# Optimization experiments

Measured on AMD Instinct MI355X. Metric: run time of the kernel, lower is better.

## Reference

```python
import jax, jax.numpy as jnp
import numpy as np

N_DIMS = 8
N_REGIMES = 8
CAPACITY = 16
KERNEL = 2
DILATIONS = (1, 2, 4, 8)
BOTTLE = (32, 32, 32, 32)
B = 128
T_LEN = 512
N_STEPS = T_LEN - CAPACITY


def setup_inputs() -> dict:
    key = jax.random.key(0)
    ks = jax.random.split(key, 8)
    x = jax.random.normal(ks[0], (B, N_DIMS, T_LEN), jnp.float32)
    temp = jnp.ones((), jnp.float32)
    u = jax.random.uniform(ks[1], (N_STEPS, B, 1, N_REGIMES), jnp.float32)

    def mkw(k, o, i):
        return jax.random.normal(k, (o, i, KERNEL), jnp.float32) / np.float32(np.sqrt(i * KERNEL))

    c_in = N_DIMS + N_REGIMES
    w0 = mkw(ks[2], BOTTLE[0], c_in)
    b0 = jnp.zeros((BOTTLE[0],), jnp.float32)
    w1 = mkw(ks[3], BOTTLE[1], BOTTLE[0])
    b1 = jnp.zeros((BOTTLE[1],), jnp.float32)
    w2 = mkw(ks[4], BOTTLE[2], BOTTLE[1])
    b2 = jnp.zeros((BOTTLE[2],), jnp.float32)
    w3 = mkw(ks[5], N_REGIMES, BOTTLE[3])
    b3 = jnp.zeros((N_REGIMES,), jnp.float32)
    return {"x": x, "temp": temp, "u": u, "w0": w0, "b0": b0, "w1": w1,
            "b1": b1, "w2": w2, "b2": b2, "w3": w3, "b3": b3, "T": T_LEN}


def _conv(h, w, b, d):
    # causal dilated conv1d, VALID padding (windowing handles causality)
    out = jax.lax.conv_general_dilated(h, w, (1,), 'VALID', rhs_dilation=(d,),
                                       dimension_numbers=('NCH', 'OIH', 'NCH'))
    return out + b[None, :, None]


def _forward(x, temp, u, params, T):
    cap = CAPACITY
    pad = sum(DILATIONS)  # F.pad(x, (sum(dilations), 0)) -> left-pad time axis
    xpad = jnp.pad(x, ((0, 0), (0, 0), (pad, 0)))
    n_steps = T - cap
    # windows x_pad[:, :, t-cap:t] for t in [cap, T) -> (n_steps, B, D, cap)
    idx = jnp.arange(n_steps)[:, None] + jnp.arange(cap)[None, :]
    xw = jnp.transpose(xpad[:, :, idx], (2, 0, 1, 3))
    g = -jnp.log(-jnp.log(u + 1e-10) + 1e-10)  # Gumbel(0,1) noise
    Bn = x.shape[0]
    K = u.shape[-1]
    z0 = jnp.zeros((Bn, K, cap), x.dtype)  # capacity initial zero regimes
    layers = tuple(zip(params[0::2], params[1::2], DILATIONS))

    def step(zbuf, inp):
        xw_t, g_t = inp  # (B, D, cap), (B, 1, K)
        h = jnp.concatenate([xw_t, zbuf], axis=1)  # (B, D+K, cap)
        for (w, b, d) in layers:
            h = jax.nn.elu(_conv(h, w, b, d))
        logq = jax.nn.log_softmax(h[:, :, -1], axis=1)  # (B, K)
        y = jax.nn.softmax((logq + g_t[:, 0, :]) / temp, axis=-1)  # gumbel-softmax sample
        zbuf = jnp.concatenate([zbuf[:, :, 1:], y[:, :, None]], axis=2)
        return zbuf, (y, logq)

    _, (zs, logqs) = jax.lax.scan(step, z0, (xw, g))
    z_all = jnp.concatenate([z0, jnp.transpose(zs, (1, 2, 0))], axis=2)  # (B, K, T)
    logq_out = jnp.transpose(logqs, (1, 2, 0))[..., None]  # (B, K, n_steps, 1) = torch.stack(dim=2)
    return z_all, logq_out


def reference(x, temp, u, w0, b0, w1, b1, w2, b2, w3, b3, T):
    return _forward(x, temp, u, (w0, b0, w1, b1, w2, b2, w3, b3), T)
```

## Files before the change

kernel.cpp:

```cpp
#include <hip/hip_runtime.h>

#define NB      128
#define ND      8
#define NK      8
#define TLEN    512
#define NSTEPS  496

#define INVLN2f 1.44269504088896340736f

__device__ __forceinline__ float fexp(float x) { return __expf(x); }
__device__ __forceinline__ float flog(float x) { return __logf(x); }
__device__ __forceinline__ float frcp(float x) { return __builtin_amdgcn_rcpf(x); }
__device__ __forceinline__ float elur(float x) { return x > 0.f ? x : fexp(x) - 1.f; }

#if defined(__has_builtin)
#if __has_builtin(__builtin_amdgcn_exp2f)
#define fexp2(x) __builtin_amdgcn_exp2f(x)
#endif
#endif
#ifndef fexp2
#define fexp2(x) exp2f(x)
#endif

#define DPP_ROR4(v) __int_as_float(__builtin_amdgcn_mov_dpp(__float_as_int(v), 0x124, 0xF, 0xF, false))
#define DPP_X1(v)   __int_as_float(__builtin_amdgcn_mov_dpp(__float_as_int(v), 0xB1, 0xF, 0xF, false))
#define DPP_X2(v)   __int_as_float(__builtin_amdgcn_mov_dpp(__float_as_int(v), 0x4E, 0xF, 0xF, false))
#define DPP_RORN(v, ctrl) __int_as_float(__builtin_amdgcn_mov_dpp(__float_as_int(v), (ctrl), 0xF, 0xF, false))

#define RED8_MAX(m) { m = fmaxf(m, DPP_X1(m)); m = fmaxf(m, DPP_X2(m)); m = fmaxf(m, DPP_ROR4(m)); }
#define RED8_SUM(s) { s = s + DPP_X1(s); s = s + DPP_X2(s); s = s + DPP_ROR4(s); }

typedef unsigned int uint2v __attribute__((ext_vector_type(2)));
typedef float floatx2 __attribute__((ext_vector_type(2)));

__device__ __forceinline__ floatx2 f2(float t) { floatx2 r; r.x = t; r.y = t; return r; }

#if defined(__has_builtin)
#if __has_builtin(__builtin_amdgcn_permlane32_swap)
#define HAVE_PLSWAP 1
#endif
#if __has_builtin(__builtin_amdgcn_permlane16_swap)
#define HAVE_PL16SWAP 1
#endif
#endif

#ifdef HAVE_PLSWAP
__device__ __forceinline__ float xhalfsum(float v) {
    unsigned int u = __float_as_uint(v);
    uint2v r = __builtin_amdgcn_permlane32_swap(u, u, false, false);
    return __uint_as_float(r[0]) + __uint_as_float(r[1]);
}
#else
__device__ __forceinline__ float xhalfsum(float v) { return v + __shfl_xor(v, 32); }
#endif

#ifdef HAVE_PL16SWAP
#define TOB(v) ({                                                                  \
    float _v = (v);                                                                \
    unsigned _u = __float_as_uint(_v);                                             \
    uint2v _r = __builtin_amdgcn_permlane16_swap(_u, _u, false, false);            \
    float _o = __uint_as_float(selr0 ? _r[0] : _r[1]);                             \
    (lane < 32) ? _v : _o; })
#else
#define TOB(v) ({                                                                  \
    float _v = (v);                                                                \
    float _o = __uint_as_float((unsigned)__builtin_amdgcn_ds_swizzle(              \
                   (int)__float_as_uint(_v), 0x401F));                             \
    (lane < 32) ? _v : _o; })
#endif

__device__ __forceinline__ floatx2 rotdot16x2p(float vB, const floatx2* __restrict__ wp) {
    float t1 = DPP_RORN(vB, 0x121), t2 = DPP_RORN(vB, 0x122), t3 = DPP_RORN(vB, 0x123);
    float t4 = DPP_RORN(vB, 0x124), t5 = DPP_RORN(vB, 0x125), t6 = DPP_RORN(vB, 0x126);
    float t7 = DPP_RORN(vB, 0x127), t8 = DPP_RORN(vB, 0x128), t9 = DPP_RORN(vB, 0x129);
    float tA = DPP_RORN(vB, 0x12A), tB = DPP_RORN(vB, 0x12B), tC = DPP_RORN(vB, 0x12C);
    float tD = DPP_RORN(vB, 0x12D), tE = DPP_RORN(vB, 0x12E), tF = DPP_RORN(vB, 0x12F);
    floatx2 a0 = wp[0] * f2(vB);
    floatx2 a1 = wp[1] * f2(t1);
    floatx2 a2 = wp[2] * f2(t2);
    floatx2 a3 = wp[3] * f2(t3);
    a0 = __builtin_elementwise_fma(wp[4],  f2(t4), a0);
    a1 = __builtin_elementwise_fma(wp[5],  f2(t5), a1);
    a2 = __builtin_elementwise_fma(wp[6],  f2(t6), a2);
    a3 = __builtin_elementwise_fma(wp[7],  f2(t7), a3);
    a0 = __builtin_elementwise_fma(wp[8],  f2(t8), a0);
    a1 = __builtin_elementwise_fma(wp[9],  f2(t9), a1);
    a2 = __builtin_elementwise_fma(wp[10], f2(tA), a2);
    a3 = __builtin_elementwise_fma(wp[11], f2(tB), a3);
    a0 = __builtin_elementwise_fma(wp[12], f2(tC), a0);
    a1 = __builtin_elementwise_fma(wp[13], f2(tD), a1);
    a2 = __builtin_elementwise_fma(wp[14], f2(tE), a2);
    a3 = __builtin_elementwise_fma(wp[15], f2(tF), a3);
    return (a0 + a1) + (a2 + a3);
}

#define STEP0(qv, S1, S2, S3, DO_OUT, XPEXPR)                                     \
  {                                                                               \
    const int q_ = (qv);                                                          \
    float o0v = elur(XZ);                                                         \
    float v0B = TOB(o0v);                                                         \
    floatx2 d1 = rotdot16x2p(v0B, w1p);                                           \
    float o1v = elur(xhalfsum(d1.x + P1[S1]));                                    \
    P1[S1] = b1h + d1.y;                                                          \
    float v1B = TOB(o1v);                                                         \
    floatx2 d2 = rotdot16x2p(v1B, w2p);                                           \
    float o2v = elur(xhalfsum(d2.x + P2[S2]));                                    \
    P2[S2] = b2h + d2.y;                                                          \
    float v2B = TOB(o2v);                                                         \
    floatx2 d3 = rotdot16x2p(v2B, w3p);                                           \
    float a3m = elur(xhalfsum(d3.x + P3[S3]));                                    \
    P3[S3] = b3h + d3.y;                                                          \
    if (DO_OUT) {                                                                 \
      amring[(q_) & 15][lane] = a3m;                                              \
      float g2_own = XGg[((q_ - 15) >> 6) & 1][(q_ - 15) & 63][o3];               \
      float F = fexp2(fmaf(a3m, klog, g2_own));                                   \
      float S = F; RED8_SUM(S);                                                   \
      float r2 = frcp(S);                                                         \
      float rt1 = DPP_RORN(F, 0x121), rt2 = DPP_RORN(F, 0x122);                   \
      float rt3 = DPP_RORN(F, 0x123), rt4 = DPP_RORN(F, 0x124);                   \
      float rt5 = DPP_RORN(F, 0x125), rt6 = DPP_RORN(F, 0x126);                   \
      float rt7 = DPP_RORN(F, 0x127);                                             \
      float na = wznrot[0] * F,   nb = wznrot[1] * rt1;                           \
      float nc = wznrot[2] * rt2, nd = wznrot[3] * rt3;                           \
      na = fmaf(wznrot[4], rt4, na); nb = fmaf(wznrot[5], rt5, nb);               \
      nc = fmaf(wznrot[6], rt6, nc); nd = fmaf(wznrot[7], rt7, nd);               \
      float oa = wzorot[0] * F,   ob = wzorot[1] * rt1;                           \
      float oc = wzorot[2] * rt2, od = wzorot[3] * rt3;                           \
      oa = fmaf(wzorot[4], rt4, oa); ob = fmaf(wzorot[5], rt5, ob);               \
      oc = fmaf(wzorot[6], rt6, oc); od = fmaf(wzorot[7], rt7, od);               \
      ZN   = ((na + nb) + (nc + nd)) * r2;                                        \
      ZQ2n = ((oa + ob) + (oc + od)) * r2;                                        \
    }                                                                             \
    XZ = ((XPEXPR) + ZQ2) + ZN;                                                   \
    ZQ2 = ZQ2n;                                                                   \
  }

#define ROLEA(pv)                                                                 \
  {                                                                               \
    const int p_ = (pv);                                                          \
    float a3 = amring[(p_) & 15][lane];                                           \
    float g2 = XGg[((p_ - 15) >> 6) & 1][(p_ - 15) & 63][o3];                     \
    float F = fexp2(fmaf(a3, klog, g2));                                          \
    float S = F; RED8_SUM(S);                                                     \
    float r2 = frcp(S);                                                           \
    float mx = a3; RED8_MAX(mx);                                                  \
    float e = fexp(a3 - mx);                                                      \
    float se = e; RED8_SUM(se);                                                   \
    float lse = mx + flog(se);                                                    \
    if (lane < 8) {                                                               \
      outg[zoff + lane * TLEN + p_ + 1]       = F * r2;                           \
      outg[qoff + lane * NSTEPS + (p_ - 15)]  = a3 - lse;                         \
    }                                                                             \
  }

__global__ __launch_bounds__(128, 1)
void regime_scan_kernel(const float* __restrict__ xg,
                        const float* __restrict__ tempg,
                        const float* __restrict__ ug,
                        const float* __restrict__ w0g,
                        const float* __restrict__ b0g,
                        const float* __restrict__ w1g,
                        const float* __restrict__ b1g,
                        const float* __restrict__ w2g,
                        const float* __restrict__ b2g,
                        const float* __restrict__ w3g,
                        const float* __restrict__ b3g,
                        float* __restrict__ outg)
{
    __shared__ __align__(16) float xring[80 * 8];
    __shared__ __align__(16) float XGx[2][64][32];
    __shared__ __align__(16) float XGg[2][64][8];
    __shared__ __align__(16) float XPwarm[15][32];
    __shared__ __align__(16) float amring[16][64];

    const int lane = threadIdx.x & 63;
    const int wid  = threadIdx.x >> 6;
    const int b    = blockIdx.x;
    const int c    = lane & 31;
    const int o3   = lane & 7;
    const int tap  = (lane < 32) ? 1 : 0;
    const int s    = lane & 15;
    const int rowq = lane >> 4;
    const int jbase = ((rowq ^ (rowq >> 1)) & 1) << 4;

    int dir;
    {
        int l15 = lane & 15;
        int rr1 = __builtin_amdgcn_mov_dpp(l15, 0x121, 0xF, 0xF, false);
        dir = (rr1 == ((l15 + 1) & 15)) ? 1 : -1;
    }
    int selr0 = 0;
#ifdef HAVE_PL16SWAP
    {
        unsigned li = (unsigned)lane;
        uint2v pr = __builtin_amdgcn_permlane16_swap(li, li, false, false);
        selr0 = (pr[0] == (li ^ 16u)) ? 1 : 0;
    }
#endif

    const float tinv = frcp(tempg[0]);
    const float klog = tinv * INVLN2f;
    const int zoff = b * (NK * TLEN);
    const int qoff = NB * NK * TLEN + b * (NK * NSTEPS);

    if (wid == 0) {
        float wznrot[8], wzorot[8];
        #pragma unroll
        for (int r = 0; r < 8; ++r) {
            int ch = (o3 + dir * r) & 7;
            wznrot[r] = w0g[c * 32 + (8 + ch) * 2 + 1];
            wzorot[r] = w0g[c * 32 + (8 + ch) * 2 + 0];
        }
        floatx2 w1p[16], w2p[16], w3p[16];
        #pragma unroll
        for (int r = 0; r < 16; ++r) {
            int jj = jbase + ((s + dir * r) & 15);
            w1p[r].x = w1g[c  * 64 + jj * 2 + 1];
            w1p[r].y = w1g[c  * 64 + jj * 2 + 0];
            w2p[r].x = w2g[c  * 64 + jj * 2 + 1];
            w2p[r].y = w2g[c  * 64 + jj * 2 + 0];
            w3p[r].x = w3g[o3 * 64 + jj * 2 + 1];
            w3p[r].y = w3g[o3 * 64 + jj * 2 + 0];
        }
        const float b1h = 0.5f * b1g[c];
        const float b2h = 0.5f * b2g[c];
        const float b3h = 0.5f * b3g[o3];

        __syncthreads();

        float P1[2] = { b1h, b1h };
        float P2[4] = { b2h, b2h, b2h, b2h };
        float P3[8];
        #pragma unroll
        for (int k = 0; k < 8; ++k) P3[k] = b3h;
        float ZQ2 = 0.f, ZQ2n = 0.f, ZN = 0.f;
        float XZ = XPwarm[1][c];

        #pragma unroll
        for (int q = 1; q <= 14; ++q) {
            STEP0(q, q & 1, q & 3, q & 7, 0,
                  (q < 14 ? XPwarm[q + 1][c] : XGx[0][0][c]));
        }
        __syncthreads();

        for (int j = 0; j < 62; ++j) {
            const int qb = 15 + 8 * j;
            #pragma unroll
            for (int u = 0; u < 8; ++u) {
                STEP0(qb + u, (15 + u) & 1, (15 + u) & 3, (15 + u) & 7, 1,
                      XGx[((qb + u - 14) >> 6) & 1][(qb + u - 14) & 63][c]);
            }
            __syncthreads();
        }
    } else {
        float wxr[8];
        #pragma unroll
        for (int d = 0; d < 8; ++d) wxr[d] = w0g[c * 32 + d * 2 + tap];
        const float b0r = b0g[c];
        const float* xb = xg + b * (ND * TLEN);

        for (int idx = lane; idx < 80 * ND; idx += 64) {
            int l = idx >> 3, d = idx & 7;
            int t = l - 15;
            xring[idx] = (t >= 0) ? xb[d * TLEN + t] : 0.f;
        }
        for (int it = 0; it <= 77; ++it) {
            const float4* xq = (const float4*)&xring[(it + tap) * 8];
            float4 xa = xq[0], xbv = xq[1];
            float s0 = fmaf(wxr[0], xa.x, fmaf(wxr[1], xa.y, 0.f));
            float s1 = fmaf(wxr[2], xa.z, fmaf(wxr[3], xa.w, 0.f));
            float s2 = fmaf(wxr[4], xbv.x, fmaf(wxr[5], xbv.y, 0.f));
            float s3 = fmaf(wxr[6], xbv.z, fmaf(wxr[7], xbv.w, 0.f));
            float h = xhalfsum((s0 + s1) + (s2 + s3)) + b0r;
            if (lane < 32) {
                if (it < 14) XPwarm[it + 1][c] = h;
                else         XGx[0][it - 14][c] = h;
            }
        }
        for (int idx = lane; idx < 64 * NK; idx += 64) {
            int st = idx >> 3, kk = idx & 7;
            float uu = ug[st * (NB * NK) + b * NK + kk];
            XGg[0][idx >> 3][kk] = -flog(-flog(uu + 1e-10f) + 1e-10f) * klog;
        }
        for (int idx = lane; idx < NK * 16; idx += 64) {
            outg[zoff + (idx >> 4) * TLEN + (idx & 15)] = 0.f;
        }

        __syncthreads();
        __syncthreads();

        for (int j = 0; j < 62; ++j) {
            if (j >= 1) {
                const int p0 = 7 + 8 * j;
                #pragma unroll
                for (int u = 0; u < 8; ++u) ROLEA(p0 + u);
            }
            if ((j & 7) == 0 && j <= 48) {
                const int cn = (j >> 3) + 1;
                const int base = 14 + 64 * cn;
                for (int idx = lane; idx < 66 * ND; idx += 64) {
                    int l = idx >> 3, d = idx & 7;
                    int t = base + l - 15;
                    xring[idx] = (t < TLEN) ? xb[d * TLEN + t] : 0.f;
                }
            }
            if ((j & 7) == 1 && j <= 49) {
                const int cn = (j >> 3) + 1;
                const int kb = cn & 1;
                for (int i = 0; i < 64; ++i) {
                    const float4* xq = (const float4*)&xring[(i + tap) * 8];
                    float4 xa = xq[0], xbv = xq[1];
                    float s0 = fmaf(wxr[0], xa.x, fmaf(wxr[1], xa.y, 0.f));
                    float s1 = fmaf(wxr[2], xa.z, fmaf(wxr[3], xa.w, 0.f));
                    float s2 = fmaf(wxr[4], xbv.x, fmaf(wxr[5], xbv.y, 0.f));
                    float s3 = fmaf(wxr[6], xbv.z, fmaf(wxr[7], xbv.w, 0.f));
                    float h = xhalfsum((s0 + s1) + (s2 + s3)) + b0r;
                    if (lane < 32) XGx[kb][i][c] = h;
                }
                for (int idx = lane; idx < 64 * NK; idx += 64) {
                    int st = 64 * cn + (idx >> 3), kk = idx & 7;
                    float v = 0.f;
                    if (st < NSTEPS) {
                        float uu = ug[st * (NB * NK) + b * NK + kk];
                        v = -flog(-flog(uu + 1e-10f) + 1e-10f) * klog;
                    }
                    XGg[kb][idx >> 3][kk] = v;
                }
            }
            __syncthreads();
        }
        {
            #pragma unroll
            for (int u = 0; u < 8; ++u) ROLEA(503 + u);
        }
    }
}

extern "C" void kernel_launch(void* const* d_in, const int* in_sizes, int n_in,
                              void* d_out, int out_size, void* d_ws, size_t ws_size,
                              hipStream_t stream) {
    (void)in_sizes; (void)n_in; (void)out_size; (void)d_ws; (void)ws_size;
    regime_scan_kernel<<<dim3(NB), dim3(128), 0, stream>>>(
        (const float*)d_in[0],
        (const float*)d_in[1],
        (const float*)d_in[2],
        (const float*)d_in[3],
        (const float*)d_in[4],
        (const float*)d_in[5],
        (const float*)d_in[6],
        (const float*)d_in[7],
        (const float*)d_in[8],
        (const float*)d_in[9],
        (const float*)d_in[10],
        (float*)d_out);
}
```

Before: 360.4 us.

## Process two batch rows per block with interleaved recurrent steps

Each block now handles two independent batch elements. Their serial recurrence steps are interleaved in one wavefront, so the latency of one chain can be hidden by the other, and the grid is halved. The 8-lane sum reduction is also rebuilt from the already computed DPP rotations instead of a separate reduction. The risk is that the longer serial loop per block, higher register pressure and only 64 blocks on a chip with many CUs could outweigh the gain from the added instruction-level parallelism.

After: 591.2 us. +64.1%, slower.

```diff
diff --git a/kernel.cpp b/kernel.cpp
--- a/kernel.cpp
+++ b/kernel.cpp
@@ -94,32 +94,33 @@
     return (a0 + a1) + (a2 + a3);
 }
 
-#define STEP0(qv, S1, S2, S3, DO_OUT, XPEXPR)                                     \
+#define STEPP(SFX, qv, S1, S2, S3, DO_OUT, XPEXPR)                                \
   {                                                                               \
     const int q_ = (qv);                                                          \
-    float o0v = elur(XZ);                                                         \
+    float o0v = elur(XZ##SFX);                                                    \
     float v0B = TOB(o0v);                                                         \
     floatx2 d1 = rotdot16x2p(v0B, w1p);                                           \
-    float o1v = elur(xhalfsum(d1.x + P1[S1]));                                    \
-    P1[S1] = b1h + d1.y;                                                          \
+    float o1v = elur(xhalfsum(d1.x + P1##SFX[S1]));                               \
+    P1##SFX[S1] = b1h + d1.y;                                                     \
     float v1B = TOB(o1v);                                                         \
     floatx2 d2 = rotdot16x2p(v1B, w2p);                                           \
-    float o2v = elur(xhalfsum(d2.x + P2[S2]));                                    \
-    P2[S2] = b2h + d2.y;                                                          \
+    float o2v = elur(xhalfsum(d2.x + P2##SFX[S2]));                               \
+    P2##SFX[S2] = b2h + d2.y;                                                     \
     float v2B = TOB(o2v);                                                         \
     floatx2 d3 = rotdot16x2p(v2B, w3p);                                           \
-    float a3m = elur(xhalfsum(d3.x + P3[S3]));                                    \
-    P3[S3] = b3h + d3.y;                                                          \
+    float a3m = elur(xhalfsum(d3.x + P3##SFX[S3]));                               \
+    P3##SFX[S3] = b3h + d3.y;                                                     \
     if (DO_OUT) {                                                                 \
-      amring[(q_) & 15][lane] = a3m;                                              \
-      float g2_own = XGg[((q_ - 15) >> 6) & 1][(q_ - 15) & 63][o3];               \
+      amr##SFX[((q_) & 15) * 64 + lane] = a3m;                                    \
+      float g2_own = xgg##SFX[((((q_) - 15) >> 6) & 1) * 512                      \
+                              + (((q_) - 15) & 63) * 8 + o3];                     \
       float F = fexp2(fmaf(a3m, klog, g2_own));                                   \
-      float S = F; RED8_SUM(S);                                                   \
-      float r2 = frcp(S);                                                         \
       float rt1 = DPP_RORN(F, 0x121), rt2 = DPP_RORN(F, 0x122);                   \
       float rt3 = DPP_RORN(F, 0x123), rt4 = DPP_RORN(F, 0x124);                   \
       float rt5 = DPP_RORN(F, 0x125), rt6 = DPP_RORN(F, 0x126);                   \
       float rt7 = DPP_RORN(F, 0x127);                                             \
+      float S = ((F + rt1) + (rt2 + rt3)) + ((rt4 + rt5) + (rt6 + rt7));          \
+      float r2 = frcp(S);                                                         \
       float na = wznrot[0] * F,   nb = wznrot[1] * rt1;                           \
       float nc = wznrot[2] * rt2, nd = wznrot[3] * rt3;                           \
       na = fmaf(wznrot[4], rt4, na); nb = fmaf(wznrot[5], rt5, nb);               \
@@ -128,28 +129,32 @@
       float oc = wzorot[2] * rt2, od = wzorot[3] * rt3;                           \
       oa = fmaf(wzorot[4], rt4, oa); ob = fmaf(wzorot[5], rt5, ob);               \
       oc = fmaf(wzorot[6], rt6, oc); od = fmaf(wzorot[7], rt7, od);               \
-      ZN   = ((na + nb) + (nc + nd)) * r2;                                        \
-      ZQ2n = ((oa + ob) + (oc + od)) * r2;                                        \
+      ZN##SFX   = ((na + nb) + (nc + nd)) * r2;                                   \
+      ZQ2n##SFX = ((oa + ob) + (oc + od)) * r2;                                   \
     }                                                                             \
-    XZ = ((XPEXPR) + ZQ2) + ZN;                                                   \
-    ZQ2 = ZQ2n;                                                                   \
+    XZ##SFX = ((XPEXPR) + ZQ2##SFX) + ZN##SFX;                                    \
+    ZQ2##SFX = ZQ2n##SFX;                                                         \
   }
 
-#define ROLEA(pv)                                                                 \
+#define ROLEA(pv, amr, xgg, zoffv, qoffv)                                         \
   {                                                                               \
     const int p_ = (pv);                                                          \
-    float a3 = amring[(p_) & 15][lane];                                           \
-    float g2 = XGg[((p_ - 15) >> 6) & 1][(p_ - 15) & 63][o3];                     \
+    float a3 = (amr)[((p_) & 15) * 64 + lane];                                    \
+    float g2 = (xgg)[(((p_ - 15) >> 6) & 1) * 512 + ((p_ - 15) & 63) * 8 + o3];   \
     float F = fexp2(fmaf(a3, klog, g2));                                          \
-    float S = F; RED8_SUM(S);                                                     \
+    float rt1 = DPP_RORN(F, 0x121), rt2 = DPP_RORN(F, 0x122);                     \
+    float rt3 = DPP_RORN(F, 0x123), rt4 = DPP_RORN(F, 0x124);                     \
+    float rt5 = DPP_RORN(F, 0x125), rt6 = DPP_RORN(F, 0x126);                     \
+    float rt7 = DPP_RORN(F, 0x127);                                               \
+    float S = ((F + rt1) + (rt2 + rt3)) + ((rt4 + rt5) + (rt6 + rt7));            \
     float r2 = frcp(S);                                                           \
     float mx = a3; RED8_MAX(mx);                                                  \
     float e = fexp(a3 - mx);                                                      \
     float se = e; RED8_SUM(se);                                                   \
     float lse = mx + flog(se);                                                    \
     if (lane < 8) {                                                               \
-      outg[zoff + lane * TLEN + p_ + 1]       = F * r2;                           \
-      outg[qoff + lane * NSTEPS + (p_ - 15)]  = a3 - lse;                         \
+      outg[(zoffv) + lane * TLEN + p_ + 1]       = F * r2;                        \
+      outg[(qoffv) + lane * NSTEPS + (p_ - 15)]  = a3 - lse;                      \
     }                                                                             \
   }
 
@@ -167,15 +172,16 @@
                         const float* __restrict__ b3g,
                         float* __restrict__ outg)
 {
-    __shared__ __align__(16) float xring[80 * 8];
-    __shared__ __align__(16) float XGx[2][64][32];
-    __shared__ __align__(16) float XGg[2][64][8];
-    __shared__ __align__(16) float XPwarm[15][32];
-    __shared__ __align__(16) float amring[16][64];
+    __shared__ __align__(16) float xring[2][80 * 8];
+    __shared__ __align__(16) float XGx[2][2][64][32];
+    __shared__ __align__(16) float XGg[2][2][64][8];
+    __shared__ __align__(16) float XPwarm[2][15][32];
+    __shared__ __align__(16) float amring[2][16][64];
 
     const int lane = threadIdx.x & 63;
     const int wid  = threadIdx.x >> 6;
-    const int b    = blockIdx.x;
+    const int bA   = blockIdx.x * 2;
+    const int bB   = bA + 1;
     const int c    = lane & 31;
     const int o3   = lane & 7;
     const int tap  = (lane < 32) ? 1 : 0;
@@ -197,11 +203,10 @@
         selr0 = (pr[0] == (li ^ 16u)) ? 1 : 0;
     }
 #endif
+    (void)s; (void)jbase; (void)dir; (void)selr0;
 
     const float tinv = frcp(tempg[0]);
     const float klog = tinv * INVLN2f;
-    const int zoff = b * (NK * TLEN);
-    const int qoff = NB * NK * TLEN + b * (NK * NSTEPS);
 
     if (wid == 0) {
         float wznrot[8], wzorot[8];
@@ -226,20 +231,31 @@
         const float b2h = 0.5f * b2g[c];
         const float b3h = 0.5f * b3g[o3];
 
+        const float* xgxA = &XGx[0][0][0][0];
+        const float* xgxB = &XGx[1][0][0][0];
+        const float* xggA = &XGg[0][0][0][0];
+        const float* xggB = &XGg[1][0][0][0];
+        float* amrA = &amring[0][0][0];
+        float* amrB = &amring[1][0][0];
+
         __syncthreads();
 
-        float P1[2] = { b1h, b1h };
-        float P2[4] = { b2h, b2h, b2h, b2h };
-        float P3[8];
-        #pragma unroll
-        for (int k = 0; k < 8; ++k) P3[k] = b3h;
-        float ZQ2 = 0.f, ZQ2n = 0.f, ZN = 0.f;
-        float XZ = XPwarm[1][c];
+        float P1A[2] = { b1h, b1h }, P1B[2] = { b1h, b1h };
+        float P2A[4] = { b2h, b2h, b2h, b2h }, P2B[4] = { b2h, b2h, b2h, b2h };
+        float P3A[8], P3B[8];
+        #pragma unroll
+        for (int k = 0; k < 8; ++k) { P3A[k] = b3h; P3B[k] = b3h; }
+        float ZQ2A = 0.f, ZQ2nA = 0.f, ZNA = 0.f;
+        float ZQ2B = 0.f, ZQ2nB = 0.f, ZNB = 0.f;
+        float XZA = XPwarm[0][1][c];
+        float XZB = XPwarm[1][1][c];
 
         #pragma unroll
         for (int q = 1; q <= 14; ++q) {
-            STEP0(q, q & 1, q & 3, q & 7, 0,
-                  (q < 14 ? XPwarm[q + 1][c] : XGx[0][0][c]));
+            STEPP(A, q, q & 1, q & 3, q & 7, 0,
+                  (q < 14 ? XPwarm[0][q + 1][c] : xgxA[c]));
+            STEPP(B, q, q & 1, q & 3, q & 7, 0,
+                  (q < 14 ? XPwarm[1][q + 1][c] : xgxB[c]));
         }
         __syncthreads();
 
@@ -247,8 +263,12 @@
             const int qb = 15 + 8 * j;
             #pragma unroll
             for (int u = 0; u < 8; ++u) {
-                STEP0(qb + u, (15 + u) & 1, (15 + u) & 3, (15 + u) & 7, 1,
-                      XGx[((qb + u - 14) >> 6) & 1][(qb + u - 14) & 63][c]);
+                STEPP(A, qb + u, (15 + u) & 1, (15 + u) & 3, (15 + u) & 7, 1,
+                      xgxA[((((qb + u) - 14) >> 6) & 1) * 2048
+                           + (((qb + u) - 14) & 63) * 32 + c]);
+                STEPP(B, qb + u, (15 + u) & 1, (15 + u) & 3, (15 + u) & 7, 1,
+                      xgxB[((((qb + u) - 14) >> 6) & 1) * 2048
+                           + (((qb + u) - 14) & 63) * 32 + c]);
             }
             __syncthreads();
         }
@@ -257,81 +277,100 @@
         #pragma unroll
         for (int d = 0; d < 8; ++d) wxr[d] = w0g[c * 32 + d * 2 + tap];
         const float b0r = b0g[c];
-        const float* xb = xg + b * (ND * TLEN);
-
-        for (int idx = lane; idx < 80 * ND; idx += 64) {
-            int l = idx >> 3, d = idx & 7;
-            int t = l - 15;
-            xring[idx] = (t >= 0) ? xb[d * TLEN + t] : 0.f;
-        }
-        for (int it = 0; it <= 77; ++it) {
-            const float4* xq = (const float4*)&xring[(it + tap) * 8];
-            float4 xa = xq[0], xbv = xq[1];
-            float s0 = fmaf(wxr[0], xa.x, fmaf(wxr[1], xa.y, 0.f));
-            float s1 = fmaf(wxr[2], xa.z, fmaf(wxr[3], xa.w, 0.f));
-            float s2 = fmaf(wxr[4], xbv.x, fmaf(wxr[5], xbv.y, 0.f));
-            float s3 = fmaf(wxr[6], xbv.z, fmaf(wxr[7], xbv.w, 0.f));
-            float h = xhalfsum((s0 + s1) + (s2 + s3)) + b0r;
-            if (lane < 32) {
-                if (it < 14) XPwarm[it + 1][c] = h;
-                else         XGx[0][it - 14][c] = h;
-            }
-        }
-        for (int idx = lane; idx < 64 * NK; idx += 64) {
-            int st = idx >> 3, kk = idx & 7;
-            float uu = ug[st * (NB * NK) + b * NK + kk];
-            XGg[0][idx >> 3][kk] = -flog(-flog(uu + 1e-10f) + 1e-10f) * klog;
-        }
-        for (int idx = lane; idx < NK * 16; idx += 64) {
-            outg[zoff + (idx >> 4) * TLEN + (idx & 15)] = 0.f;
+        const float* xbp[2]  = { xg + bA * (ND * TLEN), xg + bB * (ND * TLEN) };
+        const int    zoffs[2] = { bA * (NK * TLEN), bB * (NK * TLEN) };
+        const int    qoffs[2] = { NB * NK * TLEN + bA * (NK * NSTEPS),
+                                  NB * NK * TLEN + bB * (NK * NSTEPS) };
+
+        for (int bi = 0; bi < 2; ++bi) {
+            const float* xb = xbp[bi];
+            for (int idx = lane; idx < 80 * ND; idx += 64) {
+                int l = idx >> 3, d = idx & 7;
+                int t = l - 15;
+                xring[bi][idx] = (t >= 0) ? xb[d * TLEN + t] : 0.f;
+            }
+            for (int it = 0; it <= 77; ++it) {
+                const float4* xq = (const float4*)&xring[bi][(it + tap) * 8];
+                float4 xa = xq[0], xbv = xq[1];
+                float s0 = fmaf(wxr[0], xa.x, fmaf(wxr[1], xa.y, 0.f));
+                float s1 = fmaf(wxr[2], xa.z, fmaf(wxr[3], xa.w, 0.f));
+                float s2 = fmaf(wxr[4], xbv.x, fmaf(wxr[5], xbv.y, 0.f));
+                float s3 = fmaf(wxr[6], xbv.z, fmaf(wxr[7], xbv.w, 0.f));
+                float h = xhalfsum((s0 + s1) + (s2 + s3)) + b0r;
+                if (lane < 32) {
+                    if (it < 14) XPwarm[bi][it + 1][c] = h;
+                    else         XGx[bi][0][it - 14][c] = h;
+                }
+            }
+            for (int idx = lane; idx < 64 * NK; idx += 64) {
+                int st = idx >> 3, kk = idx & 7;
+                float uu = ug[st * (NB * NK) + (bA + bi) * NK + kk];
+                XGg[bi][0][idx >> 3][kk] = -flog(-flog(uu + 1e-10f) + 1e-10f) * klog;
+            }
+            for (int idx = lane; idx < NK * 16; idx += 64) {
+                outg[zoffs[bi] + (idx >> 4) * TLEN + (idx & 15)] = 0.f;
+            }
         }
 
         __syncthreads();
         __syncthreads();
+
+        const float* xggA = &XGg[0][0][0][0];
+        const float* xggB = &XGg[1][0][0][0];
+        const float* amrA = &amring[0][0][0];
+        const float* amrB = &amring[1][0][0];
 
         for (int j = 0; j < 62; ++j) {
             if (j >= 1) {
                 const int p0 = 7 + 8 * j;
                 #pragma unroll
-                for (int u = 0; u < 8; ++u) ROLEA(p0 + u);
-            }
-            if ((j & 7) == 0 && j <= 48) {
+                for (int u = 0; u < 8; ++u) {
+                    ROLEA(p0 + u, amrA, xggA, zoffs[0], qoffs[0]);
+                    ROLEA(p0 + u, amrB, xggB, zoffs[1], qoffs[1]);
+                }
+            }
+            const int ph = j & 7;
+            if ((ph == 0 && j <= 48) || (ph == 2 && j <= 50)) {
+                const int bi = (ph == 0) ? 0 : 1;
                 const int cn = (j >> 3) + 1;
                 const int base = 14 + 64 * cn;
+                const float* xb = xbp[bi];
                 for (int idx = lane; idx < 66 * ND; idx += 64) {
                     int l = idx >> 3, d = idx & 7;
                     int t = base + l - 15;
-                    xring[idx] = (t < TLEN) ? xb[d * TLEN + t] : 0.f;
-                }
-            }
-            if ((j & 7) == 1 && j <= 49) {
+                    xring[bi][idx] = (t < TLEN) ? xb[d * TLEN + t] : 0.f;
+                }
+            }
+            if ((ph == 1 && j <= 49) || (ph == 3 && j <= 51)) {
+                const int bi = (ph == 1) ? 0 : 1;
                 const int cn = (j >> 3) + 1;
                 const int kb = cn & 1;
                 for (int i = 0; i < 64; ++i) {
-                    const float4* xq = (const float4*)&xring[(i + tap) * 8];
+                    const float4* xq = (const float4*)&xring[bi][(i + tap) * 8];
                     float4 xa = xq[0], xbv = xq[1];
                     float s0 = fmaf(wxr[0], xa.x, fmaf(wxr[1], xa.y, 0.f));
                     float s1 = fmaf(wxr[2], xa.z, fmaf(wxr[3], xa.w, 0.f));
                     float s2 = fmaf(wxr[4], xbv.x, fmaf(wxr[5], xbv.y, 0.f));
                     float s3 = fmaf(wxr[6], xbv.z, fmaf(wxr[7], xbv.w, 0.f));
                     float h = xhalfsum((s0 + s1) + (s2 + s3)) + b0r;
-                    if (lane < 32) XGx[kb][i][c] = h;
+                    if (lane < 32) XGx[bi][kb][i][c] = h;
                 }
                 for (int idx = lane; idx < 64 * NK; idx += 64) {
                     int st = 64 * cn + (idx >> 3), kk = idx & 7;
                     float v = 0.f;
                     if (st < NSTEPS) {
-                        float uu = ug[st * (NB * NK) + b * NK + kk];
+                        float uu = ug[st * (NB * NK) + (bA + bi) * NK + kk];
                         v = -flog(-flog(uu + 1e-10f) + 1e-10f) * klog;
                     }
-                    XGg[kb][idx >> 3][kk] = v;
+                    XGg[bi][kb][idx >> 3][kk] = v;
                 }
             }
             __syncthreads();
         }
-        {
-            #pragma unroll
-            for (int u = 0; u < 8; ++u) ROLEA(503 + u);
+        #pragma unroll
+        for (int u = 0; u < 8; ++u) {
+            ROLEA(503 + u, amrA, xggA, zoffs[0], qoffs[0]);
+            ROLEA(503 + u, amrB, xggB, zoffs[1], qoffs[1]);
         }
     }
 }
@@ -340,7 +379,7 @@
                               void* d_out, int out_size, void* d_ws, size_t ws_size,
                               hipStream_t stream) {
     (void)in_sizes; (void)n_in; (void)out_size; (void)d_ws; (void)ws_size;
-    regime_scan_kernel<<<dim3(NB), dim3(128), 0, stream>>>(
+    regime_scan_kernel<<<dim3(NB / 2), dim3(128), 0, stream>>>(
         (const float*)d_in[0],
         (const float*)d_in[1],
         (const float*)d_in[2],
```
